# Kernel optimization log

Hardware: AMD Instinct MI355X
Metric: run time of the kernel (lower is better)

The kernel has to match this reference:

```python
import jax, jax.numpy as jnp
import numpy as np

B, N, D = 512, 100000, 256
MAX_K = 20
EPS = 1e-12


def setup_inputs() -> dict:
    key = jax.random.key(0)
    k1, k2, k3, k4 = jax.random.split(key, 4)
    z_ego = jax.random.normal(k1, (B, D), dtype=jnp.float32)
    exo_bank = jax.random.normal(k2, (N, D), dtype=jnp.float32)
    sim_vt = jax.random.uniform(k3, (B, N), dtype=jnp.float32)
    W = jax.random.normal(k4, (D, D), dtype=jnp.float32) / np.sqrt(D)
    return {"z_ego": z_ego, "exo_bank": exo_bank, "sim_vt": sim_vt, "W": W, "k": 16}


def _l2_normalize(x):
    # matches torch F.normalize semantics with eps clamp
    n = jnp.sqrt(jnp.sum(x * x, axis=-1, keepdims=True))
    return x / jnp.maximum(n, EPS)


def reference(z_ego, exo_bank, sim_vt, W, k):
    # bilinear projection into query space (Linear, no bias)
    q = z_ego @ W.T                              # [B, D]
    k_eff = min(int(k), MAX_K, exo_bank.shape[0])
    # pairwise cosine similarity query x bank
    sim_vv = _l2_normalize(q) @ _l2_normalize(exo_bank).T   # [B, N]
    # combined score (sim_vt already [B, N]; broadcast is identity)
    score = 0.5 * sim_vv + 0.5 * sim_vt          # [B, N]
    _, topk_idx = jax.lax.top_k(score, k_eff)    # [B, k_eff]
    gathered = exo_bank[topk_idx]                # [B, k_eff, D]
    return gathered, topk_idx
```

## Files before the change

kernel.cpp:

```cpp
#include <hip/hip_runtime.h>
#include <math.h>
#include <stdint.h>

#define B_Q    512
#define N_BANK 100000
#define D_DIM  256
#define K16    16

#define NSL    128
#define NCHUNK 1563
#define TROW   264
#define CHUNK_USHORT (64 * TROW)
#define CHUNK_BYTES  (CHUNK_USHORT * 2)
#define NGRP   6250
#define GSTRIDE 6272
#define MARGIN 5e-3f
#define CAPG   384

#define OFF_QN     0
#define OFF_QNT    0x80000
#define OFF_INORM  0x100000
#define OFF_TH     0x170000
#define OFF_GMAX   0x400000
#define OFF_BANKT  0x1400000
#define WS_NEED    ((size_t)OFF_BANKT + (size_t)NCHUNK * CHUNK_BYTES)

#define FB_OFF_INORM (B_Q * D_DIM * 4)
#define FB_OFF_PSC   (1024 * 1024)
#define FB_OFF_PID   (FB_OFF_PSC + B_Q * 128 * K16 * 4)

typedef __attribute__((ext_vector_type(8))) short short8;
typedef __attribute__((ext_vector_type(4))) float floatx4;

__device__ inline unsigned short f2bf(float x) {
    unsigned int u = __float_as_uint(x);
    unsigned int r = (u + 0x7FFFu + ((u >> 16) & 1u)) >> 16;
    return (unsigned short)r;
}
__device__ inline unsigned long long pack_key(float s, int idx) {
    unsigned int u = __float_as_uint(s);
    u ^= (u & 0x80000000u) ? 0xFFFFFFFFu : 0x80000000u;
    return ((unsigned long long)u << 32) | (unsigned int)(~(unsigned int)idx);
}
__device__ inline int key_idx(unsigned long long k) {
    return (int)(~(unsigned int)(k & 0xFFFFFFFFull));
}
__device__ inline unsigned long long shfl_down_u64(unsigned long long x, int off) {
    unsigned int lo = (unsigned int)x;
    unsigned int hi = (unsigned int)(x >> 32);
    lo = __shfl_down(lo, off, 64);
    hi = __shfl_down(hi, off, 64);
    return ((unsigned long long)hi << 32) | lo;
}
__device__ inline unsigned long long umax64(unsigned long long a, unsigned long long b) {
    return a > b ? a : b;
}


__global__ void qn_prep_kernel(const float* __restrict__ z_ego,
                               const float* __restrict__ W,
                               float* __restrict__ qn,
                               unsigned short* __restrict__ qnt) {
    __shared__ float zs[D_DIM];
    __shared__ float red[4];
    int b = blockIdx.x;
    int t = threadIdx.x;
    zs[t] = z_ego[b * D_DIM + t];
    __syncthreads();
    const float4* W4 = reinterpret_cast<const float4*>(W + (size_t)t * D_DIM);
    float acc = 0.f;
#pragma unroll 8
    for (int u = 0; u < 64; ++u) {
        float4 w = W4[u];
        acc += w.x * zs[u * 4 + 0];
        acc += w.y * zs[u * 4 + 1];
        acc += w.z * zs[u * 4 + 2];
        acc += w.w * zs[u * 4 + 3];
    }
    float ss = acc * acc;
#pragma unroll
    for (int off = 32; off > 0; off >>= 1) ss += __shfl_down(ss, off, 64);
    if ((t & 63) == 0) red[t >> 6] = ss;
    __syncthreads();
    float tot = red[0] + red[1] + red[2] + red[3];
    float n = fmaxf(sqrtf(tot), 1e-12f);
    float v = acc / n;
    qn[b * D_DIM + t] = v;
    qnt[(size_t)(b >> 6) * CHUNK_USHORT + (size_t)(b & 63) * TROW + t] = f2bf(v);
}

__global__ __launch_bounds__(256)
void prep_bank_kernel(const float* __restrict__ bank,
                      float* __restrict__ inorm,
                      unsigned short* __restrict__ bankt) {
    int c = blockIdx.x;
    int t = threadIdx.x, w = t >> 6, l = t & 63;
    unsigned short* dst = bankt + (size_t)c * CHUNK_USHORT;
#pragma unroll 1
    for (int rr = 0; rr < 16; ++rr) {
        int row = w * 16 + rr;
        int jg = c * 64 + row;
        ushort4 o = {0, 0, 0, 0};
        if (jg < N_BANK) {
            float4 v = *reinterpret_cast<const float4*>(bank + (size_t)jg * D_DIM + l * 4);
            float ss = v.x * v.x + v.y * v.y + v.z * v.z + v.w * v.w;
#pragma unroll
            for (int off = 1; off < 64; off <<= 1) ss += __shfl_xor(ss, off, 64);
            float inv = 1.0f / fmaxf(sqrtf(ss), 1e-12f);
            o.x = f2bf(v.x * inv); o.y = f2bf(v.y * inv);
            o.z = f2bf(v.z * inv); o.w = f2bf(v.w * inv);
            if (l == 0) inorm[jg] = inv;
        }
        *reinterpret_cast<ushort4*>(dst + (size_t)row * TROW + l * 4) = o;
    }
}

__global__ __launch_bounds__(256, 4)
void screen2_kernel(const unsigned short* __restrict__ qnt,
                    const unsigned short* __restrict__ bankt,
                    const float* __restrict__ svt,
                    float* __restrict__ gmax) {
    int t = threadIdx.x, w = t >> 6, l = t & 63;
    int lane16 = l & 15, quad = l >> 4;
    int qt0 = blockIdx.x & 15;
    int slice = blockIdx.x >> 4;
    int qbase = qt0 * 32;

    short8 afrag[2][8];
    {
        const unsigned short* abase = qnt + (size_t)(qt0 >> 1) * CHUNK_USHORT
                                          + (size_t)((qt0 & 1) * 32) * TROW;
#pragma unroll
        for (int s = 0; s < 2; ++s)
#pragma unroll
            for (int k = 0; k < 8; ++k)
                afrag[s][k] = *reinterpret_cast<const short8*>(
                    abase + (size_t)(16 * s + lane16) * TROW + k * 32 + quad * 8);
    }

    for (int c = slice; c < NCHUNK; c += NSL) {
        int j0 = c * 64;
        int jglob = j0 + 16 * w + lane16;
        bool inb = jglob < N_BANK;
        const unsigned short* bbase = bankt + (size_t)c * CHUNK_USHORT
                                            + (size_t)(16 * w + lane16) * TROW + quad * 8;
        float sv[2][4];
#pragma unroll
        for (int s = 0; s < 2; ++s)
#pragma unroll
            for (int r = 0; r < 4; ++r) {
                int q = qbase + 16 * s + 4 * quad + r;
                sv[s][r] = inb ? svt[(size_t)q * N_BANK + jglob] : 0.f;
            }

        floatx4 acc[2];
        acc[0] = (floatx4){0.f, 0.f, 0.f, 0.f};
        acc[1] = (floatx4){0.f, 0.f, 0.f, 0.f};
#pragma unroll
        for (int k = 0; k < 8; ++k) {
            short8 bfrag = *reinterpret_cast<const short8*>(bbase + k * 32);
            acc[0] = __builtin_amdgcn_mfma_f32_16x16x32_bf16(afrag[0][k], bfrag, acc[0], 0, 0, 0);
            acc[1] = __builtin_amdgcn_mfma_f32_16x16x32_bf16(afrag[1][k], bfrag, acc[1], 0, 0, 0);
        }

        int g = c * 4 + w;
        bool doStore = (lane16 == 0) && (g < NGRP);
#pragma unroll
        for (int s = 0; s < 2; ++s)
#pragma unroll
            for (int r = 0; r < 4; ++r) {
                float score = inb ? (0.5f * acc[s][r] + 0.5f * sv[s][r]) : -INFINITY;
                score = fmaxf(score, __shfl_xor(score, 1, 64));
                score = fmaxf(score, __shfl_xor(score, 2, 64));
                score = fmaxf(score, __shfl_xor(score, 4, 64));
                score = fmaxf(score, __shfl_xor(score, 8, 64));
                if (doStore) {
                    int q = qbase + 16 * s + 4 * quad + r;
                    gmax[(size_t)q * GSTRIDE + g] = score;
                }
            }
    }
}

__global__ __launch_bounds__(256)
void gthresh_kernel(const float* __restrict__ gmax,
                    float* __restrict__ th) {
    __shared__ float buf[NGRP];
    __shared__ float red[4];
    int q = blockIdx.x, t = threadIdx.x, w = t >> 6;
    for (int i = t; i < NGRP; i += 256) buf[i] = gmax[(size_t)q * GSTRIDE + i];
    __syncthreads();
    float s16 = -INFINITY;
    for (int r = 0; r < K16; ++r) {
        float m = -INFINITY;
        for (int i = t; i < NGRP; i += 256) m = fmaxf(m, buf[i]);
#pragma unroll
        for (int off = 32; off > 0; off >>= 1) m = fmaxf(m, __shfl_down(m, off, 64));
        if ((t & 63) == 0) red[w] = m;
        __syncthreads();
        m = fmaxf(fmaxf(red[0], red[1]), fmaxf(red[2], red[3]));
        if (r == K16 - 1) s16 = m;
        if (r < K16 - 1) {
            for (int i = t; i < NGRP; i += 256)
                if (buf[i] == m) buf[i] = -INFINITY;
        }
        __syncthreads();
    }
    if (t == 0) th[q] = s16 - MARGIN;
}

__global__ __launch_bounds__(256)
void grescore_kernel(const float* __restrict__ gmax,
                     const float* __restrict__ th,
                     const float* __restrict__ qn,
                     const float* __restrict__ inorm,
                     const float* __restrict__ bank,
                     const float* __restrict__ svt,
                     float* __restrict__ out) {
    __shared__ float qns[D_DIM];
    __shared__ int glist[CAPG];
    __shared__ unsigned long long keys2[CAPG * K16];
    __shared__ unsigned long long wred[4];
    __shared__ int winI[K16];
    __shared__ int gcntS;
    int b = blockIdx.x, t = threadIdx.x;
    int w = t >> 6, l = t & 63;

    qns[t] = qn[(size_t)b * D_DIM + t];
    if (t == 0) gcntS = 0;
    __syncthreads();
    float thb = th[b];
    for (int g = t; g < NGRP; g += 256) {
        if (gmax[(size_t)b * GSTRIDE + g] >= thb) {
            int p = atomicAdd(&gcntS, 1);
            if (p < CAPG) glist[p] = g;
        }
    }
    __syncthreads();
    int ng = gcntS < CAPG ? gcntS : CAPG;
    int ncand = ng * K16;

    const float4* bank4 = reinterpret_cast<const float4*>(bank);
    float4 qv = reinterpret_cast<const float4*>(qns)[l];
    for (int ci = w; ci < ncand; ci += 4) {
        int j = glist[ci >> 4] * K16 + (ci & 15);
        float4 bv = bank4[(size_t)j * 64 + l];
        float d = qv.x * bv.x + qv.y * bv.y + qv.z * bv.z + qv.w * bv.w;
#pragma unroll
        for (int off = 32; off > 0; off >>= 1) d += __shfl_down(d, off, 64);
        if (l == 0) {
            float score = 0.5f * (d * inorm[j]) + 0.5f * svt[(size_t)b * N_BANK + j];
            keys2[ci] = pack_key(score, j);
        }
    }
    __syncthreads();

    for (int r = 0; r < K16; ++r) {
        unsigned long long best = 0ull;
        for (int i = t; i < ncand; i += 256) best = umax64(best, keys2[i]);
#pragma unroll
        for (int off = 32; off > 0; off >>= 1) best = umax64(best, shfl_down_u64(best, off));
        if (l == 0) wred[w] = best;
        __syncthreads();
        unsigned long long W = umax64(umax64(wred[0], wred[1]), umax64(wred[2], wred[3]));
        if (t == 0) winI[r] = key_idx(W);
        for (int i = t; i < ncand; i += 256)
            if (keys2[i] == W) keys2[i] = 0ull;
        __syncthreads();
    }

    if (t < K16)
        out[(size_t)B_Q * K16 * D_DIM + (size_t)b * K16 + t] = (float)winI[t];
    float4* out4 = reinterpret_cast<float4*>(out);
    for (int u = t; u < K16 * 64; u += 256) {
        int r = u >> 6, cc = u & 63;
        out4[((size_t)b * K16 + r) * 64 + cc] = bank4[(size_t)winI[r] * 64 + cc];
    }
}

#define FBT 64
#define FJT 64
#define FKC 64
#define FNS 128
#define FNC ((N_BANK + FJT - 1) / FJT)

__global__ void inorm_kernel(const float* __restrict__ bank,
                             float* __restrict__ inorm) {
    int w = threadIdx.x >> 6;
    int lane = threadIdx.x & 63;
    int j = blockIdx.x * 4 + w;
    if (j >= N_BANK) return;
    const float4* r4 = reinterpret_cast<const float4*>(bank + (size_t)j * D_DIM);
    float4 v = r4[lane];
    float ss = v.x * v.x + v.y * v.y + v.z * v.z + v.w * v.w;
#pragma unroll
    for (int off = 32; off > 0; off >>= 1) ss += __shfl_down(ss, off, 64);
    if (lane == 0) inorm[j] = 1.0f / fmaxf(sqrtf(ss), 1e-12f);
}

__global__ void fb_qn_kernel(const float* __restrict__ z_ego,
                             const float* __restrict__ W,
                             float* __restrict__ qn) {
    __shared__ float zs[D_DIM];
    __shared__ float red[4];
    int b = blockIdx.x;
    int t = threadIdx.x;
    zs[t] = z_ego[b * D_DIM + t];
    __syncthreads();
    const float4* W4 = reinterpret_cast<const float4*>(W + (size_t)t * D_DIM);
    float acc = 0.f;
#pragma unroll 8
    for (int u = 0; u < 64; ++u) {
        float4 w = W4[u];
        acc += w.x * zs[u * 4 + 0]; acc += w.y * zs[u * 4 + 1];
        acc += w.z * zs[u * 4 + 2]; acc += w.w * zs[u * 4 + 3];
    }
    float ss = acc * acc;
#pragma unroll
    for (int off = 32; off > 0; off >>= 1) ss += __shfl_down(ss, off, 64);
    if ((t & 63) == 0) red[t >> 6] = ss;
    __syncthreads();
    float tot = red[0] + red[1] + red[2] + red[3];
    qn[b * D_DIM + t] = acc / fmaxf(sqrtf(tot), 1e-12f);
}

__global__ __launch_bounds__(256)
void fb_score_topk_kernel(const float* __restrict__ qn,
                          const float* __restrict__ bank,
                          const float* __restrict__ svt,
                          const float* __restrict__ inorm,
                          float* __restrict__ psc,
                          int* __restrict__ pid) {
    __shared__ float As[FKC][FBT];
    __shared__ float Bsh[FKC][FJT];
    __shared__ float Ss[FBT][FJT + 1];
    int slice = blockIdx.x;
    int qbase = blockIdx.y * FBT;
    int t = threadIdx.x;
    int tq = t >> 4, tj = t & 15;
    int q0 = tq * 4, j0l = tj * 4;
    float sc[K16]; int id[K16];
#pragma unroll
    for (int i = 0; i < K16; ++i) { sc[i] = -INFINITY; id[i] = 0x7fffffff; }
    for (int c = slice; c < FNC; c += FNS) {
        int j0 = c * FJT;
        float acc[4][4];
#pragma unroll
        for (int a = 0; a < 4; ++a)
#pragma unroll
            for (int b2 = 0; b2 < 4; ++b2) acc[a][b2] = 0.f;
        for (int kc = 0; kc < D_DIM; kc += FKC) {
            __syncthreads();
#pragma unroll
            for (int r = 0; r < 4; ++r) {
                int idx = t + 256 * r;
                int q = idx & 63, kv = idx >> 6;
                float4 v = *reinterpret_cast<const float4*>(
                    &qn[(size_t)(qbase + q) * D_DIM + kc + kv * 4]);
                As[kv * 4 + 0][q] = v.x; As[kv * 4 + 1][q] = v.y;
                As[kv * 4 + 2][q] = v.z; As[kv * 4 + 3][q] = v.w;
            }
#pragma unroll
            for (int r = 0; r < 4; ++r) {
                int idx = t + 256 * r;
                int j = idx & 63, kv = idx >> 6;
                int jg = j0 + j;
                float4 v = make_float4(0.f, 0.f, 0.f, 0.f);
                if (jg < N_BANK)
                    v = *reinterpret_cast<const float4*>(
                        &bank[(size_t)jg * D_DIM + kc + kv * 4]);
                Bsh[kv * 4 + 0][j] = v.x; Bsh[kv * 4 + 1][j] = v.y;
                Bsh[kv * 4 + 2][j] = v.z; Bsh[kv * 4 + 3][j] = v.w;
            }
            __syncthreads();
#pragma unroll
            for (int k = 0; k < FKC; ++k) {
                float4 av = *reinterpret_cast<const float4*>(&As[k][q0]);
                float4 bv = *reinterpret_cast<const float4*>(&Bsh[k][j0l]);
                float a[4] = {av.x, av.y, av.z, av.w};
                float bb[4] = {bv.x, bv.y, bv.z, bv.w};
#pragma unroll
                for (int qi = 0; qi < 4; ++qi)
#pragma unroll
                    for (int ji = 0; ji < 4; ++ji) acc[qi][ji] += a[qi] * bb[ji];
            }
        }
        bool full = (j0 + FJT <= N_BANK);
        if (full) {
            float4 inv = *reinterpret_cast<const float4*>(&inorm[j0 + j0l]);
            float iv[4] = {inv.x, inv.y, inv.z, inv.w};
#pragma unroll
            for (int qi = 0; qi < 4; ++qi) {
                int q = qbase + q0 + qi;
                float4 svv = *reinterpret_cast<const float4*>(
                    &svt[(size_t)q * N_BANK + j0 + j0l]);
                float s[4] = {svv.x, svv.y, svv.z, svv.w};
#pragma unroll
                for (int ji = 0; ji < 4; ++ji)
                    Ss[q0 + qi][j0l + ji] = 0.5f * (acc[qi][ji] * iv[ji]) + 0.5f * s[ji];
            }
        } else {
#pragma unroll
            for (int qi = 0; qi < 4; ++qi) {
                int q = qbase + q0 + qi;
#pragma unroll
                for (int ji = 0; ji < 4; ++ji) {
                    int jg = j0 + j0l + ji;
                    float s = -INFINITY;
                    if (jg < N_BANK)
                        s = 0.5f * (acc[qi][ji] * inorm[jg]) + 0.5f * svt[(size_t)q * N_BANK + jg];
                    Ss[q0 + qi][j0l + ji] = s;
                }
            }
        }
        __syncthreads();
        if (t < FBT) {
#pragma unroll 1
            for (int jj = 0; jj < FJT; ++jj) {
                int jg = j0 + jj;
                if (jg >= N_BANK) break;
                float s = Ss[t][jj];
                if (s > sc[K16 - 1] || (s == sc[K16 - 1] && jg < id[K16 - 1])) {
                    float cs = s; int ci = jg;
#pragma unroll
                    for (int i = 0; i < K16; ++i) {
                        bool bt2 = (cs > sc[i]) || (cs == sc[i] && ci < id[i]);
                        float ts = sc[i]; int ti = id[i];
                        if (bt2) { sc[i] = cs; id[i] = ci; cs = ts; ci = ti; }
                    }
                }
            }
        }
    }
    if (t < FBT) {
        int q = qbase + t;
        size_t base = ((size_t)q * FNS + slice) * K16;
#pragma unroll
        for (int i = 0; i < K16; ++i) { psc[base + i] = sc[i]; pid[base + i] = id[i]; }
    }
}

__global__ __launch_bounds__(256)
void fb_merge_kernel(const float* __restrict__ psc,
                     const int* __restrict__ pid,
                     const float* __restrict__ bank,
                     float* __restrict__ out) {
    __shared__ unsigned long long keys[FNS * K16];
    __shared__ unsigned long long wred[4];
    __shared__ int win[K16];
    int b = blockIdx.x, t = threadIdx.x;
    for (int i = t; i < FNS * K16; i += 256) {
        float s = psc[(size_t)b * FNS * K16 + i];
        unsigned int u = __float_as_uint(s);
        u ^= (u & 0x80000000u) ? 0xFFFFFFFFu : 0x80000000u;
        unsigned int iv = ~(unsigned int)pid[(size_t)b * FNS * K16 + i];
        keys[i] = ((unsigned long long)u << 32) | iv;
    }
    __syncthreads();
    for (int r = 0; r < K16; ++r) {
        unsigned long long best = 0ull;
        for (int i = t; i < FNS * K16; i += 256) best = umax64(best, keys[i]);
#pragma unroll
        for (int off = 32; off > 0; off >>= 1) best = umax64(best, shfl_down_u64(best, off));
        if ((t & 63) == 0) wred[t >> 6] = best;
        __syncthreads();
        unsigned long long w = umax64(umax64(wred[0], wred[1]), umax64(wred[2], wred[3]));
        if (t == 0) win[r] = (int)(~(unsigned int)w);
        for (int i = t; i < FNS * K16; i += 256)
            if (keys[i] == w) keys[i] = 0ull;
        __syncthreads();
    }
    if (t < K16)
        out[(size_t)B_Q * K16 * D_DIM + (size_t)b * K16 + t] = (float)win[t];
    const float4* bank4 = reinterpret_cast<const float4*>(bank);
    float4* out4 = reinterpret_cast<float4*>(out);
    for (int u = t; u < K16 * 64; u += 256) {
        int r = u >> 6, c = u & 63;
        out4[((size_t)b * K16 + r) * 64 + c] = bank4[(size_t)win[r] * 64 + c];
    }
}

extern "C" void kernel_launch(void* const* d_in, const int* in_sizes, int n_in,
                              void* d_out, int out_size, void* d_ws, size_t ws_size,
                              hipStream_t stream) {
    const float* z_ego = (const float*)d_in[0];
    const float* bank  = (const float*)d_in[1];
    const float* svt   = (const float*)d_in[2];
    const float* W     = (const float*)d_in[3];
    float* out = (float*)d_out;
    char* ws = (char*)d_ws;

    if (ws_size >= WS_NEED) {
        float* qn             = (float*)(ws + OFF_QN);
        unsigned short* qnt   = (unsigned short*)(ws + OFF_QNT);
        float* inorm          = (float*)(ws + OFF_INORM);
        float* th             = (float*)(ws + OFF_TH);
        float* gmax           = (float*)(ws + OFF_GMAX);
        unsigned short* bankt = (unsigned short*)(ws + OFF_BANKT);

        qn_prep_kernel<<<B_Q, 256, 0, stream>>>(z_ego, W, qn, qnt);
        prep_bank_kernel<<<NCHUNK, 256, 0, stream>>>(bank, inorm, bankt);
        screen2_kernel<<<NSL * 16, 256, 0, stream>>>(qnt, bankt, svt, gmax);
        gthresh_kernel<<<B_Q, 256, 0, stream>>>(gmax, th);
        grescore_kernel<<<B_Q, 256, 0, stream>>>(gmax, th, qn, inorm, bank, svt, out);
    } else {
        float* qn    = (float*)(ws + 0);
        float* inorm = (float*)(ws + FB_OFF_INORM);
        float* psc   = (float*)(ws + FB_OFF_PSC);
        int*   pid   = (int*)(ws + FB_OFF_PID);
        fb_qn_kernel<<<B_Q, 256, 0, stream>>>(z_ego, W, qn);
        inorm_kernel<<<(N_BANK + 3) / 4, 256, 0, stream>>>(bank, inorm);
        dim3 grid(FNS, B_Q / FBT);
        fb_score_topk_kernel<<<grid, 256, 0, stream>>>(qn, bank, svt, inorm, psc, pid);
        fb_merge_kernel<<<B_Q, 256, 0, stream>>>(psc, pid, bank, out);
    }
}
```

Before: 731.9 us.

## Stage bank chunks in LDS via async global_load_lds and reassign waves to query tiles

The screening kernel now loads each 64-row bank chunk into shared memory with async global-to-LDS loads. Each of the four waves works on a different 32-query tile, so a chunk is fetched once per block for 128 queries instead of once per 32-query tile. Blocks are mapped to slices so that all 4 query blocks of a slice share an XCD. The sim_vt reads are software-prefetched one 16-column group ahead. This cuts the L2/HBM traffic for the bf16 bank but adds LDS use and two barriers per chunk, which may limit occupancy.

```diff
diff --git a/kernel.cpp b/kernel.cpp
--- a/kernel.cpp
+++ b/kernel.cpp
@@ -7,7 +7,7 @@
 #define D_DIM  256
 #define K16    16
 
-#define NSL    128
+#define NSL2   256
 #define NCHUNK 1563
 #define TROW   264
 #define CHUNK_USHORT (64 * TROW)
@@ -31,6 +31,9 @@
 
 typedef __attribute__((ext_vector_type(8))) short short8;
 typedef __attribute__((ext_vector_type(4))) float floatx4;
+
+typedef __attribute__((address_space(1))) const unsigned char gu8_t;
+typedef __attribute__((address_space(3))) unsigned char lu8_t;
 
 __device__ inline unsigned short f2bf(float x) {
     unsigned int u = __float_as_uint(x);
@@ -116,20 +119,27 @@
 }
 
 __global__ __launch_bounds__(256, 4)
-void screen2_kernel(const unsigned short* __restrict__ qnt,
+void screen3_kernel(const unsigned short* __restrict__ qnt,
                     const unsigned short* __restrict__ bankt,
                     const float* __restrict__ svt,
                     float* __restrict__ gmax) {
+    __shared__ unsigned short lbank[CHUNK_USHORT];
     int t = threadIdx.x, w = t >> 6, l = t & 63;
     int lane16 = l & 15, quad = l >> 4;
-    int qt0 = blockIdx.x & 15;
-    int slice = blockIdx.x >> 4;
-    int qbase = qt0 * 32;
+
+    int bid = blockIdx.x;
+    int xcd = bid & 7;
+    int t2 = bid >> 3;
+    int qb = t2 & 3;
+    int slice = xcd + 8 * (t2 >> 2);
+
+    int qt = qb * 4 + w;
+    int qbase = qt * 32;
 
     short8 afrag[2][8];
     {
-        const unsigned short* abase = qnt + (size_t)(qt0 >> 1) * CHUNK_USHORT
-                                          + (size_t)((qt0 & 1) * 32) * TROW;
+        const unsigned short* abase = qnt + (size_t)(qt >> 1) * CHUNK_USHORT
+                                          + (size_t)((qt & 1) * 32) * TROW;
 #pragma unroll
         for (int s = 0; s < 2; ++s)
 #pragma unroll
@@ -138,47 +148,96 @@
                     abase + (size_t)(16 * s + lane16) * TROW + k * 32 + quad * 8);
     }
 
-    for (int c = slice; c < NCHUNK; c += NSL) {
+    const float* svr[2][4];
+#pragma unroll
+    for (int s = 0; s < 2; ++s)
+#pragma unroll
+        for (int r = 0; r < 4; ++r)
+            svr[s][r] = svt + (size_t)(qbase + 16 * s + 4 * quad + r) * (size_t)N_BANK;
+
+    for (int c = slice; c < NCHUNK; c += NSL2) {
         int j0 = c * 64;
-        int jglob = j0 + 16 * w + lane16;
-        bool inb = jglob < N_BANK;
-        const unsigned short* bbase = bankt + (size_t)c * CHUNK_USHORT
-                                            + (size_t)(16 * w + lane16) * TROW + quad * 8;
-        float sv[2][4];
-#pragma unroll
-        for (int s = 0; s < 2; ++s)
-#pragma unroll
-            for (int r = 0; r < 4; ++r) {
-                int q = qbase + 16 * s + 4 * quad + r;
-                sv[s][r] = inb ? svt[(size_t)q * N_BANK + jglob] : 0.f;
-            }
-
-        floatx4 acc[2];
-        acc[0] = (floatx4){0.f, 0.f, 0.f, 0.f};
-        acc[1] = (floatx4){0.f, 0.f, 0.f, 0.f};
-#pragma unroll
-        for (int k = 0; k < 8; ++k) {
-            short8 bfrag = *reinterpret_cast<const short8*>(bbase + k * 32);
-            acc[0] = __builtin_amdgcn_mfma_f32_16x16x32_bf16(afrag[0][k], bfrag, acc[0], 0, 0, 0);
-            acc[1] = __builtin_amdgcn_mfma_f32_16x16x32_bf16(afrag[1][k], bfrag, acc[1], 0, 0, 0);
-        }
-
-        int g = c * 4 + w;
-        bool doStore = (lane16 == 0) && (g < NGRP);
-#pragma unroll
-        for (int s = 0; s < 2; ++s)
-#pragma unroll
-            for (int r = 0; r < 4; ++r) {
-                float score = inb ? (0.5f * acc[s][r] + 0.5f * sv[s][r]) : -INFINITY;
-                score = fmaxf(score, __shfl_xor(score, 1, 64));
-                score = fmaxf(score, __shfl_xor(score, 2, 64));
-                score = fmaxf(score, __shfl_xor(score, 4, 64));
-                score = fmaxf(score, __shfl_xor(score, 8, 64));
-                if (doStore) {
-                    int q = qbase + 16 * s + 4 * quad + r;
-                    gmax[(size_t)q * GSTRIDE + g] = score;
+
+        {
+            const unsigned char* gsrc = (const unsigned char*)bankt + (size_t)c * CHUNK_BYTES;
+            unsigned char* lbase = (unsigned char*)lbank;
+#pragma unroll
+            for (int i = 0; i < 8; ++i) {
+                int off = i * 4096 + w * 1024;
+                __builtin_amdgcn_global_load_lds((gu8_t*)(gsrc + off + l * 16),
+                                                 (lu8_t*)(lbase + off), 16, 0, 0);
+            }
+            int off8 = 32768 + w * 256;
+            __builtin_amdgcn_global_load_lds((gu8_t*)(gsrc + off8 + l * 4),
+                                             (lu8_t*)(lbase + off8), 4, 0, 0);
+        }
+
+        float sv_cur[2][4], sv_nxt[2][4];
+        {
+            int jglob = j0 + lane16;
+            bool inb = jglob < N_BANK;
+#pragma unroll
+            for (int s = 0; s < 2; ++s)
+#pragma unroll
+                for (int r = 0; r < 4; ++r)
+                    sv_cur[s][r] = inb ? svr[s][r][jglob] : 0.f;
+        }
+
+        __syncthreads();
+
+        int g0 = c * 4;
+#pragma unroll
+        for (int jg = 0; jg < 4; ++jg) {
+            if (jg < 3) {
+                int jglob = j0 + 16 * (jg + 1) + lane16;
+                bool inb = jglob < N_BANK;
+#pragma unroll
+                for (int s = 0; s < 2; ++s)
+#pragma unroll
+                    for (int r = 0; r < 4; ++r)
+                        sv_nxt[s][r] = inb ? svr[s][r][jglob] : 0.f;
+            }
+
+            floatx4 acc0 = (floatx4){0.f, 0.f, 0.f, 0.f};
+            floatx4 acc1 = (floatx4){0.f, 0.f, 0.f, 0.f};
+            const unsigned short* bbase = lbank + (size_t)(16 * jg + lane16) * TROW + quad * 8;
+#pragma unroll
+            for (int k = 0; k < 8; ++k) {
+                short8 bfrag = *reinterpret_cast<const short8*>(bbase + k * 32);
+                acc0 = __builtin_amdgcn_mfma_f32_16x16x32_bf16(afrag[0][k], bfrag, acc0, 0, 0, 0);
+                acc1 = __builtin_amdgcn_mfma_f32_16x16x32_bf16(afrag[1][k], bfrag, acc1, 0, 0, 0);
+            }
+
+            int jglob = j0 + 16 * jg + lane16;
+            bool inb = jglob < N_BANK;
+            int g = g0 + jg;
+            bool doStore = (lane16 == 0) && (g < NGRP);
+#pragma unroll
+            for (int s = 0; s < 2; ++s) {
+#pragma unroll
+                for (int r = 0; r < 4; ++r) {
+                    float a = (s == 0) ? acc0[r] : acc1[r];
+                    float score = inb ? (0.5f * a + 0.5f * sv_cur[s][r]) : -INFINITY;
+                    score = fmaxf(score, __shfl_xor(score, 1, 64));
+                    score = fmaxf(score, __shfl_xor(score, 2, 64));
+                    score = fmaxf(score, __shfl_xor(score, 4, 64));
+                    score = fmaxf(score, __shfl_xor(score, 8, 64));
+                    if (doStore) {
+                        int q = qbase + 16 * s + 4 * quad + r;
+                        gmax[(size_t)q * GSTRIDE + g] = score;
+                    }
                 }
             }
+
+            if (jg < 3) {
+#pragma unroll
+                for (int s = 0; s < 2; ++s)
+#pragma unroll
+                    for (int r = 0; r < 4; ++r)
+                        sv_cur[s][r] = sv_nxt[s][r];
+            }
+        }
+        __syncthreads();
     }
 }
 
@@ -500,7 +559,7 @@
 
         qn_prep_kernel<<<B_Q, 256, 0, stream>>>(z_ego, W, qn, qnt);
         prep_bank_kernel<<<NCHUNK, 256, 0, stream>>>(bank, inorm, bankt);
-        screen2_kernel<<<NSL * 16, 256, 0, stream>>>(qnt, bankt, svt, gmax);
+        screen3_kernel<<<NSL2 * 4, 256, 0, stream>>>(qnt, bankt, svt, gmax);
         gthresh_kernel<<<B_Q, 256, 0, stream>>>(gmax, th);
         grescore_kernel<<<B_Q, 256, 0, stream>>>(gmax, th, qn, inorm, bank, svt, out);
     } else {
```

Result: no change. 726.2 us (-0.8%).
